# Performance work log

Hardware: AMD Instinct MI355X
Metric: run time of the kernel (lower is better)

The kernel has to match this reference:

```python
import jax, jax.numpy as jnp
import numpy as np

B, L, D = 2, 2048, 512
NUM_HEADS = 8
LN_EPS = 1e-5


def setup_inputs() -> dict:
    key = jax.random.key(0)
    ks = jax.random.split(key, 4)
    s = 1.0 / np.sqrt(D)
    return {
        "x": jax.random.normal(ks[0], (B, L, D), dtype=jnp.float32),
        "in_proj_w": jax.random.normal(ks[1], (3 * D, D), dtype=jnp.float32) * s,
        "in_proj_b": jnp.zeros((3 * D,), dtype=jnp.float32),
        "out_proj_w": jax.random.normal(ks[2], (D, D), dtype=jnp.float32) * s,
        "out_proj_b": jnp.zeros((D,), dtype=jnp.float32),
        "ln_gamma": jnp.ones((D,), dtype=jnp.float32),
        "ln_beta": jnp.zeros((D,), dtype=jnp.float32),
        "window_size": 10,
    }


def reference(x, in_proj_w, in_proj_b, out_proj_w, out_proj_b, ln_gamma, ln_beta, window_size):
    b, l, d = x.shape
    h = NUM_HEADS
    hd = d // h

    # packed qkv projection (torch Linear: y = x @ W.T + b)
    qkv = x @ in_proj_w.T + in_proj_b  # [B, L, 3D]
    q, k, v = jnp.split(qkv, 3, axis=-1)

    def heads(t):  # [B, L, D] -> [B, H, L, hd]
        return t.reshape(b, l, h, hd).transpose(0, 2, 1, 3)

    q, k, v = heads(q), heads(k), heads(v)
    q = q * (1.0 / np.sqrt(hd))  # torch MHA scales q

    scores = jnp.einsum("bhqd,bhkd->bhqk", q, k)  # [B, H, L, L]

    # Faithful to the source + torch bool attn_mask semantics:
    # mask starts all-True, positions OUTSIDE window set to False;
    # torch masks (=-inf) where the bool mask is True, i.e. INSIDE
    # the window [i - w//2, i + w//2).
    half = window_size // 2
    i = jnp.arange(l)[:, None]
    j = jnp.arange(l)[None, :]
    banned = (j >= i - half) & (j < i + half)  # [L, L] bool
    scores = jnp.where(banned[None, None], -jnp.inf, scores)

    attn = jax.nn.softmax(scores, axis=-1)
    ctx = jnp.einsum("bhqk,bhkd->bhqd", attn, v)  # [B, H, L, hd]
    ctx = ctx.transpose(0, 2, 1, 3).reshape(b, l, d)
    attn_out = ctx @ out_proj_w.T + out_proj_b

    # residual + LayerNorm
    y = x + attn_out
    mu = jnp.mean(y, axis=-1, keepdims=True)
    var = jnp.mean(jnp.square(y - mu), axis=-1, keepdims=True)
    return (y - mu) * jax.lax.rsqrt(var + LN_EPS) * ln_gamma + ln_beta
```

## Files before the change

### kernel.cpp

```cpp
#include <hip/hip_runtime.h>
#include <hip/hip_bf16.h>
#include <math.h>

namespace {

constexpr int Bb = 2, Ll = 2048, Dd = 512, Hh = 8;
constexpr int M = Bb * Ll;
constexpr int THREE_D = 3 * Dd;

typedef __attribute__((ext_vector_type(8))) short short8;
typedef __attribute__((ext_vector_type(4))) short short4v;
typedef __attribute__((ext_vector_type(4))) float f32x4;

__device__ __forceinline__ unsigned short f2bf(float x) {
  union { __hip_bfloat16 h; unsigned short u; } cv;
  cv.h = __float2bfloat16(x);
  return cv.u;
}

__device__ __forceinline__ void gload_lds16(const void* g, void* l) {
  __builtin_amdgcn_global_load_lds(
      (const __attribute__((address_space(1))) void*)g,
      (__attribute__((address_space(3))) void*)l, 16, 0, 0);
}

constexpr int QUADS_X = (M * Dd) / 4;
constexpr int QUADS_W1 = (THREE_D * Dd) / 4;
constexpr int QUADS_W2 = (Dd * Dd) / 4;
constexpr int QUADS_TOT = QUADS_X + QUADS_W1 + QUADS_W2;

__global__ __launch_bounds__(256) void cvt_bf16(
    const float* __restrict__ x, const float* __restrict__ w1,
    const float* __restrict__ w2, unsigned short* __restrict__ xb,
    unsigned short* __restrict__ wb, unsigned short* __restrict__ wob) {
  const int i = blockIdx.x * 256 + threadIdx.x;
  const float* src;
  unsigned short* dst;
  if (i < QUADS_X) {
    src = x + 4 * (size_t)i;
    dst = xb + 4 * (size_t)i;
  } else if (i < QUADS_X + QUADS_W1) {
    const int j = i - QUADS_X;
    src = w1 + 4 * (size_t)j;
    dst = wb + 4 * (size_t)j;
  } else {
    const int j = i - (QUADS_X + QUADS_W1);
    src = w2 + 4 * (size_t)j;
    dst = wob + 4 * (size_t)j;
  }
  float4 v = *reinterpret_cast<const float4*>(src);
  ushort4 o;
  o.x = f2bf(v.x); o.y = f2bf(v.y); o.z = f2bf(v.z); o.w = f2bf(v.w);
  *reinterpret_cast<ushort4*>(dst) = o;
}

template <int K, int N, bool QKV>
__global__ __launch_bounds__(256) void gemm_mfma(
    const unsigned short* __restrict__ A, const unsigned short* __restrict__ B,
    const float* __restrict__ bias, const float* __restrict__ R,
    unsigned short* __restrict__ Cb, float* __restrict__ Cf) {
  __shared__ unsigned short As[128 * 64];
  __shared__ unsigned short Bs[128 * 64];

  const int tid = threadIdx.x;
  const int lane = tid & 63;
  const int wu = __builtin_amdgcn_readfirstlane(tid >> 6);
  const int q = lane & 15;
  const int g = lane >> 4;
  const int wr = wu >> 1, wc = wu & 1;
  const int m0 = blockIdx.y * 128, n0 = blockIdx.x * 128;

  const int srow = lane >> 3;
  const int scol = 8 * ((lane & 7) ^ srow);
  const unsigned short* Ag = A + (size_t)(m0 + 32 * wu + srow) * K + scol;
  const unsigned short* Bg = B + (size_t)(n0 + 32 * wu + srow) * K + scol;
  char* AsW = (char*)As + wu * 4096;
  char* BsW = (char*)Bs + wu * 4096;

  f32x4 acc[4][4] = {};

  for (int k0 = 0; k0 < K; k0 += 64) {
    __syncthreads();
#pragma unroll
    for (int i = 0; i < 4; ++i) {
      gload_lds16(Ag + (size_t)(8 * i) * K + k0, AsW + 1024 * i);
      gload_lds16(Bg + (size_t)(8 * i) * K + k0, BsW + 1024 * i);
    }
    __syncthreads();

    const char* Abase = (const char*)As + (wr * 64 + q) * 128;
    const char* Bbase = (const char*)Bs + (wc * 64 + q) * 128;
#pragma unroll
    for (int s = 0; s < 2; ++s) {
      const int csw = (64 * s + 16 * g) ^ ((q & 7) << 4);
      short8 af[4], bf[4];
#pragma unroll
      for (int m = 0; m < 4; ++m)
        af[m] = *reinterpret_cast<const short8*>(Abase + m * 2048 + csw);
#pragma unroll
      for (int n = 0; n < 4; ++n)
        bf[n] = *reinterpret_cast<const short8*>(Bbase + n * 2048 + csw);
#pragma unroll
      for (int m = 0; m < 4; ++m)
#pragma unroll
        for (int n = 0; n < 4; ++n)
          acc[m][n] = __builtin_amdgcn_mfma_f32_16x16x32_bf16(
              af[m], bf[n], acc[m][n], 0, 0, 0);
    }
  }

  const float sc = (QKV && n0 < Dd) ? 0.125f : 1.0f;
#pragma unroll
  for (int m = 0; m < 4; ++m) {
#pragma unroll
    for (int r = 0; r < 4; ++r) {
      const int row = m0 + wr * 64 + m * 16 + 4 * g + r;
#pragma unroll
      for (int n = 0; n < 4; ++n) {
        const int col = n0 + wc * 64 + n * 16 + q;
        const float v = acc[m][n][r] + bias[col];
        if (QKV) {
          Cb[(size_t)row * N + col] = f2bf(v * sc);
        } else {
          Cf[(size_t)row * N + col] = v + R[(size_t)row * N + col];
        }
      }
    }
  }
}

__global__ __launch_bounds__(512) void attn_mfma(
    const unsigned short* __restrict__ qkv, const int* __restrict__ wsz,
    unsigned short* __restrict__ ctx) {
  __shared__ unsigned short Kls[16384];
  __shared__ unsigned short Vls[8192];
  __shared__ unsigned short Pls[8192];

  const int tid = threadIdx.x;
  const int lane = tid & 63;
  const int w = tid >> 6;
  const int wu = __builtin_amdgcn_readfirstlane(w);
  const int wg = wu & 3;
  const int hv = wu >> 2;
  const int q = lane & 15;
  const int g = lane >> 4;

  const int qt = blockIdx.x & 31;
  const int h = (blockIdx.x >> 5) & 7;
  const int b = blockIdx.x >> 8;
  const int qbase = qt * 64;
  const int hwin = wsz[0] >> 1;

  const size_t bh_base = (size_t)b * Ll * THREE_D + h * 64;

  const unsigned short* qrow =
      qkv + bh_base + (size_t)(qbase + wg * 16 + q) * THREE_D;
  short8 qf0 = *reinterpret_cast<const short8*>(qrow + 8 * g);
  short8 qf1 = *reinterpret_cast<const short8*>(qrow + 32 + 8 * g);
  asm volatile("s_waitcnt vmcnt(0)" : "+v"(qf0), "+v"(qf1)::"memory");

  const int k_rowoff = wg * 16 + (lane >> 3);
  const int k_dcol = 8 * ((lane & 7) ^ ((lane >> 3) & 7));
  const unsigned short* kg_base = qkv + bh_base + Dd + k_dcol;

  const int v_rowoff = 32 * (wg >> 1) + 8 * ((lane >> 4) & 3) +
                       4 * ((lane >> 3) & 1) + ((lane >> 1) & 3);
  const unsigned short* vg_base = qkv + bh_base + 2 * Dd + 8 * (lane & 1);

  unsigned short* kst = &Kls[hv * 8192 + wg * 1024];
  unsigned short* vst = &Vls[hv * 4096 + wg * 1024];
  unsigned short* pw = &Pls[wu * 1024];
  const char* vbytes = (const char*)Vls + hv * 8192;
  char* pb = (char*)pw;

  f32x4 oacc[4] = {};
  float m_run = -1e30f, l_run = 0.f;

  const int qlo = qbase + wg * 16;
  const int iq = qlo + q;
  const int kb0 = hv * 1024;

  gload_lds16(kg_base + (size_t)(kb0 + k_rowoff) * THREE_D, kst);
  gload_lds16(kg_base + (size_t)(kb0 + k_rowoff + 8) * THREE_D, kst + 512);
  gload_lds16(vg_base + (size_t)(kb0 + v_rowoff) * THREE_D +
                  16 * ((2 * wg + 0) & 3), vst);
  gload_lds16(vg_base + (size_t)(kb0 + v_rowoff) * THREE_D +
                  16 * ((2 * wg + 1) & 3), vst + 512);

  for (int t = 0; t < 16; ++t) {
    const int kbase = (hv * 16 + t) * 64;
    const int cur = t & 1;

    if (t < 15) {
      unsigned short* kd = kst + (cur ^ 1) * 4096;
      gload_lds16(kg_base + (size_t)(kbase + 64 + k_rowoff) * THREE_D, kd);
      gload_lds16(kg_base + (size_t)(kbase + 64 + k_rowoff + 8) * THREE_D,
                  kd + 512);
      asm volatile("s_waitcnt vmcnt(4)" ::: "memory");
    } else {
      asm volatile("s_waitcnt vmcnt(2)" ::: "memory");
    }
    __builtin_amdgcn_s_barrier();

    f32x4 sa[4] = {};
    const char* kbytes = (const char*)Kls + hv * 16384 + cur * 8192;
    __builtin_amdgcn_s_setprio(1);
#pragma unroll
    for (int s = 0; s < 2; ++s) {
      const short8 qf = s ? qf1 : qf0;
#pragma unroll
      for (int n = 0; n < 4; ++n) {
        const int baddr =
            (((16 * n + q) * 128 + 64 * s + 16 * g)) ^ ((q & 7) << 4);
        const short8 kf = *reinterpret_cast<const short8*>(kbytes + baddr);
        sa[n] = __builtin_amdgcn_mfma_f32_16x16x32_bf16(kf, qf, sa[n], 0, 0, 0);
      }
    }
    __builtin_amdgcn_s_setprio(0);

    if (kbase + 64 > qlo - hwin && kbase < qlo + 15 + hwin) {
#pragma unroll
      for (int n = 0; n < 4; ++n) {
#pragma unroll
        for (int r = 0; r < 4; ++r) {
          const int j = kbase + 16 * n + 4 * g + r;
          if (j >= iq - hwin && j < iq + hwin) sa[n][r] = -1e30f;
        }
      }
    }

    const float mx0 = fmaxf(fmaxf(sa[0][0], sa[0][1]), fmaxf(sa[0][2], sa[0][3]));
    const float mx1 = fmaxf(fmaxf(sa[1][0], sa[1][1]), fmaxf(sa[1][2], sa[1][3]));
    const float mx2 = fmaxf(fmaxf(sa[2][0], sa[2][1]), fmaxf(sa[2][2], sa[2][3]));
    const float mx3 = fmaxf(fmaxf(sa[3][0], sa[3][1]), fmaxf(sa[3][2], sa[3][3]));
    float mx = fmaxf(fmaxf(mx0, mx1), fmaxf(mx2, mx3));
    mx = fmaxf(mx, __shfl_xor(mx, 16));
    mx = fmaxf(mx, __shfl_xor(mx, 32));
    const float mnew = fmaxf(m_run, mx);
    const float corr = __expf(m_run - mnew);
    m_run = mnew;
#pragma unroll
    for (int n = 0; n < 4; ++n)
#pragma unroll
      for (int r = 0; r < 4; ++r) sa[n][r] = __expf(sa[n][r] - mnew);
    const float s0 = (sa[0][0] + sa[0][1]) + (sa[0][2] + sa[0][3]);
    const float s1 = (sa[1][0] + sa[1][1]) + (sa[1][2] + sa[1][3]);
    const float s2 = (sa[2][0] + sa[2][1]) + (sa[2][2] + sa[2][3]);
    const float s3 = (sa[3][0] + sa[3][1]) + (sa[3][2] + sa[3][3]);
    float ps = (s0 + s1) + (s2 + s3);
    ps += __shfl_xor(ps, 16);
    ps += __shfl_xor(ps, 32);
    l_run = l_run * corr + ps;

    float corr_o[4];
#pragma unroll
    for (int r = 0; r < 4; ++r) corr_o[r] = __shfl(corr, 4 * g + r, 16);
#pragma unroll
    for (int n = 0; n < 4; ++n)
#pragma unroll
      for (int r = 0; r < 4; ++r) oacc[n][r] *= corr_o[r];

#pragma unroll
    for (int n = 0; n < 4; ++n) {
      uint2 pk;
      pk.x = (unsigned)f2bf(sa[n][0]) | ((unsigned)f2bf(sa[n][1]) << 16);
      pk.y = (unsigned)f2bf(sa[n][2]) | ((unsigned)f2bf(sa[n][3]) << 16);
      *reinterpret_cast<uint2*>(
          pb + q * 128 + ((32 * n + 8 * g) ^ ((q & 7) << 4))) = pk;
    }
    asm volatile("s_waitcnt lgkmcnt(0)" ::: "memory");

    if (t < 15) asm volatile("s_waitcnt vmcnt(2)" ::: "memory");
    else        asm volatile("s_waitcnt vmcnt(0)" ::: "memory");
    __builtin_amdgcn_s_barrier();

#pragma unroll
    for (int s = 0; s < 2; ++s) {
      const short8 pf = *reinterpret_cast<const short8*>(
          pb + q * 128 + ((64 * s + 16 * g) ^ ((q & 7) << 4)));
      short4v vlo[4], vhi[4];
#pragma unroll
      for (int n = 0; n < 4; ++n) {
        const __attribute__((address_space(3))) unsigned short* va =
            (const __attribute__((address_space(3))) unsigned short*)(
                vbytes + 4096 * s + 1024 * n + 256 * g + 8 * q);
        asm volatile("ds_read_b64_tr_b16 %0, %1 offset:0" : "=v"(vlo[n]) : "v"(va));
        asm volatile("ds_read_b64_tr_b16 %0, %1 offset:128" : "=v"(vhi[n]) : "v"(va));
      }
      asm volatile("s_waitcnt lgkmcnt(0)"
                   : "+v"(vlo[0]), "+v"(vhi[0]), "+v"(vlo[1]), "+v"(vhi[1]),
                     "+v"(vlo[2]), "+v"(vhi[2]), "+v"(vlo[3]), "+v"(vhi[3])
                   :
                   : "memory");
      __builtin_amdgcn_sched_barrier(0);
      __builtin_amdgcn_s_setprio(1);
#pragma unroll
      for (int n = 0; n < 4; ++n) {
        const short8 vf =
            __builtin_shufflevector(vlo[n], vhi[n], 0, 1, 2, 3, 4, 5, 6, 7);
        oacc[n] = __builtin_amdgcn_mfma_f32_16x16x32_bf16(pf, vf, oacc[n], 0, 0, 0);
      }
      __builtin_amdgcn_s_setprio(0);
    }

    __builtin_amdgcn_s_barrier();

    if (t < 15) {
      gload_lds16(vg_base + (size_t)(kbase + 64 + v_rowoff) * THREE_D +
                      16 * ((2 * wg + 0) & 3), vst);
      gload_lds16(vg_base + (size_t)(kbase + 64 + v_rowoff) * THREE_D +
                      16 * ((2 * wg + 1) & 3), vst + 512);
    }
  }

  float* Om = (float*)Kls;
  float* mls = (float*)Vls;

  __syncthreads();
  if (w >= 4) {
#pragma unroll
    for (int r = 0; r < 4; ++r) {
      const int rr = wg * 16 + 4 * g + r;
#pragma unroll
      for (int n = 0; n < 4; ++n) Om[rr * 64 + 16 * n + q] = oacc[n][r];
    }
    if (g == 0)
      *reinterpret_cast<float2*>(&mls[(wg * 16 + q) * 2]) =
          make_float2(m_run, l_run);
  }
  __syncthreads();
  if (w < 4) {
#pragma unroll
    for (int r = 0; r < 4; ++r) {
      const int rr = wg * 16 + 4 * g + r;
      const float m_own = __shfl(m_run, 4 * g + r, 16);
      const float l_own = __shfl(l_run, 4 * g + r, 16);
      const float2 ml2 = *reinterpret_cast<const float2*>(&mls[rr * 2]);
      const float ms = fmaxf(m_own, ml2.x);
      const float c1 = __expf(m_own - ms);
      const float c2 = __expf(ml2.x - ms);
      const float inv = 1.0f / (c1 * l_own + c2 * ml2.y);
      const int row = qbase + rr;
      unsigned short* crow = ctx + ((size_t)(b * Ll + row)) * Dd + h * 64 + q;
#pragma unroll
      for (int n = 0; n < 4; ++n) {
        const float o2 = Om[rr * 64 + 16 * n + q];
        crow[16 * n] = f2bf((c1 * oacc[n][r] + c2 * o2) * inv);
      }
    }
  }
}

__global__ __launch_bounds__(256) void ln_kernel(
    const float* __restrict__ y, const float* __restrict__ gamma,
    const float* __restrict__ beta, float* __restrict__ out) {
  const int row = blockIdx.x;
  const int tid = threadIdx.x;
  const float* yr = y + (size_t)row * Dd;

  float2 v = *reinterpret_cast<const float2*>(&yr[tid * 2]);
  float s = v.x + v.y;
  float qq = v.x * v.x + v.y * v.y;
#pragma unroll
  for (int off = 1; off < 64; off <<= 1) {
    s += __shfl_xor(s, off, 64);
    qq += __shfl_xor(qq, off, 64);
  }
  __shared__ float ss[4], qs[4];
  if ((tid & 63) == 0) { ss[tid >> 6] = s; qs[tid >> 6] = qq; }
  __syncthreads();
  s = (ss[0] + ss[1]) + (ss[2] + ss[3]);
  qq = (qs[0] + qs[1]) + (qs[2] + qs[3]);

  const float mu = s * (1.0f / Dd);
  const float var = qq * (1.0f / Dd) - mu * mu;
  const float rstd = rsqrtf(var + 1e-5f);

  float2 gmv = *reinterpret_cast<const float2*>(&gamma[tid * 2]);
  float2 bev = *reinterpret_cast<const float2*>(&beta[tid * 2]);
  float2 o;
  o.x = (v.x - mu) * rstd * gmv.x + bev.x;
  o.y = (v.y - mu) * rstd * gmv.y + bev.y;
  *reinterpret_cast<float2*>(&out[(size_t)row * Dd + tid * 2]) = o;
}

}

extern "C" void kernel_launch(void* const* d_in, const int* in_sizes, int n_in,
                              void* d_out, int out_size, void* d_ws,
                              size_t ws_size, hipStream_t stream) {
  const float* x = (const float*)d_in[0];
  const float* w_in = (const float*)d_in[1];
  const float* b_in = (const float*)d_in[2];
  const float* w_out = (const float*)d_in[3];
  const float* b_out = (const float*)d_in[4];
  const float* gamma = (const float*)d_in[5];
  const float* beta = (const float*)d_in[6];
  const int* wsz = (const int*)d_in[7];
  float* out = (float*)d_out;

  unsigned short* ws16 = (unsigned short*)d_ws;
  unsigned short* qkvb = ws16;
  unsigned short* ctxb = ws16 + 6291456;
  unsigned short* xb = ws16 + 8388608;
  unsigned short* wb = ws16 + 10485760;
  unsigned short* wob = ws16 + 11272192;
  float* y = (float*)d_ws;

  dim3 blk(256);

  cvt_bf16<<<dim3(QUADS_TOT / 256), blk, 0, stream>>>(x, w_in, w_out, xb, wb,
                                                      wob);
  gemm_mfma<512, 1536, true><<<dim3(12, 32), blk, 0, stream>>>(
      xb, wb, b_in, nullptr, qkvb, nullptr);
  attn_mfma<<<dim3(512), dim3(512), 0, stream>>>(qkvb, wsz, ctxb);
  gemm_mfma<512, 512, false><<<dim3(4, 32), blk, 0, stream>>>(
      ctxb, wob, b_out, x, nullptr, y);
  ln_kernel<<<dim3(M), blk, 0, stream>>>(y, gamma, beta, out);
}
```

Baseline: 82.84 us.

## Replace double-buffered K/V prefetch with synchronous per-tile loads in attention

The attention kernel's software pipeline is removed. K is no longer double-buffered and the next V tile is no longer prefetched at the end of each iteration. Instead, each iteration loads its own K and V tile between two __syncthreads barriers. This halves the K shared-memory buffer, cutting LDS use, and simplifies the barrier and vmcnt bookkeeping. In exchange, global-memory latency for every tile is fully exposed before the QK^T MFMAs can start, unless the lower LDS footprint lets more blocks overlap on a CU.

```diff
diff --git a/kernel.cpp b/kernel.cpp
--- a/kernel.cpp
+++ b/kernel.cpp
@@ -132,7 +132,7 @@
 __global__ __launch_bounds__(512) void attn_mfma(
     const unsigned short* __restrict__ qkv, const int* __restrict__ wsz,
     unsigned short* __restrict__ ctx) {
-  __shared__ unsigned short Kls[16384];
+  __shared__ unsigned short Kls[8192];
   __shared__ unsigned short Vls[8192];
   __shared__ unsigned short Pls[8192];
 
@@ -167,9 +167,10 @@
                        4 * ((lane >> 3) & 1) + ((lane >> 1) & 3);
   const unsigned short* vg_base = qkv + bh_base + 2 * Dd + 8 * (lane & 1);
 
-  unsigned short* kst = &Kls[hv * 8192 + wg * 1024];
+  unsigned short* kst = &Kls[hv * 4096 + wg * 1024];
   unsigned short* vst = &Vls[hv * 4096 + wg * 1024];
   unsigned short* pw = &Pls[wu * 1024];
+  const char* kbytes = (const char*)Kls + hv * 8192;
   const char* vbytes = (const char*)Vls + hv * 8192;
   char* pb = (char*)pw;
 
@@ -178,32 +179,20 @@
 
   const int qlo = qbase + wg * 16;
   const int iq = qlo + q;
-  const int kb0 = hv * 1024;
-
-  gload_lds16(kg_base + (size_t)(kb0 + k_rowoff) * THREE_D, kst);
-  gload_lds16(kg_base + (size_t)(kb0 + k_rowoff + 8) * THREE_D, kst + 512);
-  gload_lds16(vg_base + (size_t)(kb0 + v_rowoff) * THREE_D +
-                  16 * ((2 * wg + 0) & 3), vst);
-  gload_lds16(vg_base + (size_t)(kb0 + v_rowoff) * THREE_D +
-                  16 * ((2 * wg + 1) & 3), vst + 512);
 
   for (int t = 0; t < 16; ++t) {
     const int kbase = (hv * 16 + t) * 64;
-    const int cur = t & 1;
-
-    if (t < 15) {
-      unsigned short* kd = kst + (cur ^ 1) * 4096;
-      gload_lds16(kg_base + (size_t)(kbase + 64 + k_rowoff) * THREE_D, kd);
-      gload_lds16(kg_base + (size_t)(kbase + 64 + k_rowoff + 8) * THREE_D,
-                  kd + 512);
-      asm volatile("s_waitcnt vmcnt(4)" ::: "memory");
-    } else {
-      asm volatile("s_waitcnt vmcnt(2)" ::: "memory");
-    }
-    __builtin_amdgcn_s_barrier();
+    __syncthreads();
+
+    gload_lds16(kg_base + (size_t)(kbase + k_rowoff) * THREE_D, kst);
+    gload_lds16(kg_base + (size_t)(kbase + k_rowoff + 8) * THREE_D, kst + 512);
+    gload_lds16(vg_base + (size_t)(kbase + v_rowoff) * THREE_D +
+                    16 * ((2 * wg + 0) & 3), vst);
+    gload_lds16(vg_base + (size_t)(kbase + v_rowoff) * THREE_D +
+                    16 * ((2 * wg + 1) & 3), vst + 512);
+    __syncthreads();
 
     f32x4 sa[4] = {};
-    const char* kbytes = (const char*)Kls + hv * 16384 + cur * 8192;
     __builtin_amdgcn_s_setprio(1);
 #pragma unroll
     for (int s = 0; s < 2; ++s) {
@@ -270,10 +259,6 @@
     }
     asm volatile("s_waitcnt lgkmcnt(0)" ::: "memory");
 
-    if (t < 15) asm volatile("s_waitcnt vmcnt(2)" ::: "memory");
-    else        asm volatile("s_waitcnt vmcnt(0)" ::: "memory");
-    __builtin_amdgcn_s_barrier();
-
 #pragma unroll
     for (int s = 0; s < 2; ++s) {
       const short8 pf = *reinterpret_cast<const short8*>(
@@ -301,15 +286,6 @@
         oacc[n] = __builtin_amdgcn_mfma_f32_16x16x32_bf16(pf, vf, oacc[n], 0, 0, 0);
       }
       __builtin_amdgcn_s_setprio(0);
-    }
-
-    __builtin_amdgcn_s_barrier();
-
-    if (t < 15) {
-      gload_lds16(vg_base + (size_t)(kbase + 64 + v_rowoff) * THREE_D +
-                      16 * ((2 * wg + 0) & 3), vst);
-      gload_lds16(vg_base + (size_t)(kbase + 64 + v_rowoff) * THREE_D +
-                      16 * ((2 * wg + 1) & 3), vst + 512);
     }
   }
 
```

New measurement: 80.37 us. -3.0%, faster.
